# Kernel tuning notes

Hardware: AMD Instinct MI355X
Metric: run time of the kernel (lower is better)

The kernel has to match this reference:

```python
import jax, jax.numpy as jnp
import numpy as np


def setup_inputs() -> dict:
    key = jax.random.key(0)
    k1, k2 = jax.random.split(key)
    N = 2_000_000
    rotation = jax.random.normal(k1, (N, 3, 3), dtype=jnp.float32)
    # learned parameter: eye(3) + 0.001 * randn(3,3)
    mat = jnp.eye(3, dtype=jnp.float32) + 0.001 * jax.random.normal(k2, (3, 3), dtype=jnp.float32)
    return {"rotation": rotation, "mat": mat}


def reference(rotation, mat):
    # new_mat[n] = rotation[n] @ mat   (mat broadcast over the batch)
    new_mat = jnp.einsum('nab,bc->nac', rotation, mat)
    # batched 3x3 SVD; polar orthogonal factor U @ V^T
    U, S, Vh = jnp.linalg.svd(new_mat, full_matrices=False)
    out = jnp.einsum('nab,nbc->nac', U, Vh)  # Vh is already V^T
    logdet = jnp.zeros((rotation.shape[0],), dtype=rotation.dtype)
    return out, logdet
```

## Files before the change

### kernel.cpp

```cpp
#include <hip/hip_runtime.h>
#include <math.h>

constexpr int BLOCK = 256;

__global__ __launch_bounds__(BLOCK) void polar3x3_kernel(
    const float* __restrict__ rot,
    const float* __restrict__ mat,
    float* __restrict__ outq,
    float* __restrict__ logdet,
    int N)
{
    __shared__ float lds[BLOCK * 9];
    const int tid = threadIdx.x;
    const long long base = (long long)blockIdx.x * BLOCK;
    const int rem = (int)(N - base);
    const int nmat = rem < BLOCK ? rem : BLOCK;
    const int nflt = nmat * 9;
    const int nv4 = nflt >> 2;

    const float* gsrc = rot + base * 9;
    {
        const float4* g4 = (const float4*)gsrc;
        float4* l4 = (float4*)lds;
        for (int i = tid; i < nv4; i += BLOCK) l4[i] = g4[i];
        for (int i = (nv4 << 2) + tid; i < nflt; i += BLOCK) lds[i] = gsrc[i];
    }

    const float m0=mat[0], m1=mat[1], m2=mat[2], m3=mat[3], m4=mat[4],
                m5=mat[5], m6=mat[6], m7=mat[7], m8=mat[8];
    const double dM = (double)m0*((double)m4*m8-(double)m5*m7)
                    - (double)m1*((double)m3*m8-(double)m5*m6)
                    + (double)m2*((double)m3*m7-(double)m4*m6);
    __syncthreads();

    const bool active = tid < nmat;
    float x0=1.f,x1=0.f,x2=0.f,x3=0.f,x4=1.f,x5=0.f,x6=0.f,x7=0.f,x8=1.f;
    float detA = 1.f;

    if (active) {
        const float* r = &lds[tid * 9];
        const float r0=r[0],r1=r[1],r2=r[2],r3=r[3],r4=r[4],r5=r[5],r6=r[6],r7=r[7],r8=r[8];
        const double dR = (double)r0*((double)r4*r8-(double)r5*r7)
                        - (double)r1*((double)r3*r8-(double)r5*r6)
                        + (double)r2*((double)r3*r7-(double)r4*r6);
        detA = (float)(dR * dM);
        x0=fmaf(r0,m0,fmaf(r1,m3,r2*m6));
        x1=fmaf(r0,m1,fmaf(r1,m4,r2*m7));
        x2=fmaf(r0,m2,fmaf(r1,m5,r2*m8));
        x3=fmaf(r3,m0,fmaf(r4,m3,r5*m6));
        x4=fmaf(r3,m1,fmaf(r4,m4,r5*m7));
        x5=fmaf(r3,m2,fmaf(r4,m5,r5*m8));
        x6=fmaf(r6,m0,fmaf(r7,m3,r8*m6));
        x7=fmaf(r6,m1,fmaf(r7,m4,r8*m7));
        x8=fmaf(r6,m2,fmaf(r7,m5,r8*m8));
    }

    #pragma unroll
    for (int it = 0; it < 5; ++it) {
        const float c0=fmaf(x4,x8,-x5*x7), c1=fmaf(x5,x6,-x3*x8), c2=fmaf(x3,x7,-x4*x6);
        const float c3=fmaf(x2,x7,-x1*x8), c4=fmaf(x0,x8,-x2*x6), c5=fmaf(x1,x6,-x0*x7);
        const float c6=fmaf(x1,x5,-x2*x4), c7=fmaf(x2,x3,-x0*x5), c8=fmaf(x0,x4,-x1*x3);
        const float det = (it==0) ? detA : fmaf(x0,c0,fmaf(x1,c1,x2*c2));
        const float adet = fmaxf(fabsf(det), 1e-30f);
        float nX2, nC2;
        { const float a=fmaf(x1,x1,x0*x0), b=fmaf(x3,x3,x2*x2),
                      e=fmaf(x5,x5,x4*x4), d=fmaf(x7,x7,x6*x6);
          nX2=(a+b)+(e+fmaf(x8,x8,d)); }
        { const float a=fmaf(c1,c1,c0*c0), b=fmaf(c3,c3,c2*c2),
                      e=fmaf(c5,c5,c4*c4), d=fmaf(c7,c7,c6*c6);
          nC2=(a+b)+(e+fmaf(c8,c8,d)); }
        const float h  = __builtin_amdgcn_rsqf(adet);
        const float pr = __builtin_amdgcn_sqrtf(__builtin_amdgcn_sqrtf(
                             nC2*__builtin_amdgcn_rcpf(nX2)));
        const float qr = __builtin_amdgcn_sqrtf(__builtin_amdgcn_sqrtf(
                             nX2*__builtin_amdgcn_rcpf(nC2)));
        const float s = 0.5f*pr*h;
        const float t = copysignf(0.5f*qr*h, det);
        x0=fmaf(s,x0,t*c0); x1=fmaf(s,x1,t*c1); x2=fmaf(s,x2,t*c2);
        x3=fmaf(s,x3,t*c3); x4=fmaf(s,x4,t*c4); x5=fmaf(s,x5,t*c5);
        x6=fmaf(s,x6,t*c6); x7=fmaf(s,x7,t*c7); x8=fmaf(s,x8,t*c8);
    }
    {
        const float c0=fmaf(x4,x8,-x5*x7), c1=fmaf(x5,x6,-x3*x8), c2=fmaf(x3,x7,-x4*x6);
        const float c3=fmaf(x2,x7,-x1*x8), c4=fmaf(x0,x8,-x2*x6), c5=fmaf(x1,x6,-x0*x7);
        const float c6=fmaf(x1,x5,-x2*x4), c7=fmaf(x2,x3,-x0*x5), c8=fmaf(x0,x4,-x1*x3);
        const float det = fmaf(x0,c0,fmaf(x1,c1,x2*c2));
        const float t = 0.5f*__builtin_amdgcn_rcpf(det);
        x0=fmaf(0.5f,x0,t*c0); x1=fmaf(0.5f,x1,t*c1); x2=fmaf(0.5f,x2,t*c2);
        x3=fmaf(0.5f,x3,t*c3); x4=fmaf(0.5f,x4,t*c4); x5=fmaf(0.5f,x5,t*c5);
        x6=fmaf(0.5f,x6,t*c6); x7=fmaf(0.5f,x7,t*c7); x8=fmaf(0.5f,x8,t*c8);
    }

    if (active) {
        float* w = &lds[tid * 9];
        w[0]=x0; w[1]=x1; w[2]=x2; w[3]=x3; w[4]=x4;
        w[5]=x5; w[6]=x6; w[7]=x7; w[8]=x8;
    }
    __syncthreads();

    float* gdst = outq + base * 9;
    {
        float4* g4 = (float4*)gdst;
        const float4* l4 = (const float4*)lds;
        for (int i = tid; i < nv4; i += BLOCK) g4[i] = l4[i];
        for (int i = (nv4 << 2) + tid; i < nflt; i += BLOCK) gdst[i] = lds[i];
    }

    if (base + tid < N) logdet[base + tid] = 0.0f;
}

extern "C" void kernel_launch(void* const* d_in, const int* in_sizes, int n_in,
                              void* d_out, int out_size, void* d_ws, size_t ws_size,
                              hipStream_t stream) {
    const float* rot = (const float*)d_in[0];
    const float* mat = (const float*)d_in[1];
    float* out = (float*)d_out;
    const int N = in_sizes[0] / 9;
    float* logdet = out + (long long)N * 9;
    const int nblocks = (N + BLOCK - 1) / BLOCK;
    polar3x3_kernel<<<nblocks, BLOCK, 0, stream>>>(rot, mat, out, logdet, N);
}
```

Measured before the change: 138.8 us.

## Use per-wave LDS staging, fp32 determinants, and drop final Newton step

Each wave now stages its own 64 matrices through LDS with wave barriers instead of block-wide __syncthreads. Tail handling is removed, so it assumes N is a multiple of 64. Determinants are computed in fp32, falling back to fp64 only when the value is near zero. The per-iteration scaling needs fewer transcendental calls, and the final unscaled Newton iteration is removed, which may cost accuracy.

New measurement: 145.6 us. +4.9%, slower.

```diff
diff --git a/kernel.cpp b/kernel.cpp
--- a/kernel.cpp
+++ b/kernel.cpp
@@ -2,6 +2,7 @@
 #include <math.h>
 
 constexpr int BLOCK = 256;
+constexpr int WAVE  = 64;
 
 __global__ __launch_bounds__(BLOCK) void polar3x3_kernel(
     const float* __restrict__ rot,
@@ -11,49 +12,52 @@
     int N)
 {
     __shared__ float lds[BLOCK * 9];
-    const int tid = threadIdx.x;
-    const long long base = (long long)blockIdx.x * BLOCK;
-    const int rem = (int)(N - base);
-    const int nmat = rem < BLOCK ? rem : BLOCK;
-    const int nflt = nmat * 9;
-    const int nv4 = nflt >> 2;
+    const int tid  = threadIdx.x;
+    const int lane = tid & 63;
+    const int wave = tid >> 6;
+    const long long matBase = (long long)blockIdx.x * BLOCK + (long long)wave * WAVE;
+    if (matBase >= N) return;
 
-    const float* gsrc = rot + base * 9;
+    float* wlds = &lds[wave * (WAVE * 9)];
+
     {
-        const float4* g4 = (const float4*)gsrc;
-        float4* l4 = (float4*)lds;
-        for (int i = tid; i < nv4; i += BLOCK) l4[i] = g4[i];
-        for (int i = (nv4 << 2) + tid; i < nflt; i += BLOCK) lds[i] = gsrc[i];
+        const float4* g4 = (const float4*)(rot + matBase * 9);
+        float4* l4 = (float4*)wlds;
+        l4[lane]      = g4[lane];
+        l4[lane + 64] = g4[lane + 64];
+        if (lane < 16) l4[lane + 128] = g4[lane + 128];
     }
+    __builtin_amdgcn_wave_barrier();
 
     const float m0=mat[0], m1=mat[1], m2=mat[2], m3=mat[3], m4=mat[4],
                 m5=mat[5], m6=mat[6], m7=mat[7], m8=mat[8];
-    const double dM = (double)m0*((double)m4*m8-(double)m5*m7)
-                    - (double)m1*((double)m3*m8-(double)m5*m6)
-                    + (double)m2*((double)m3*m7-(double)m4*m6);
-    __syncthreads();
+    const float dMf = fmaf(m0, fmaf(m4,m8,-m5*m7),
+                      fmaf(-m1, fmaf(m3,m8,-m5*m6),
+                           m2 * fmaf(m3,m7,-m4*m6)));
 
-    const bool active = tid < nmat;
-    float x0=1.f,x1=0.f,x2=0.f,x3=0.f,x4=1.f,x5=0.f,x6=0.f,x7=0.f,x8=1.f;
-    float detA = 1.f;
+    const float* r = &wlds[lane * 9];
+    const float r0=r[0],r1=r[1],r2=r[2],r3=r[3],r4=r[4],r5=r[5],r6=r[6],r7=r[7],r8=r[8];
 
-    if (active) {
-        const float* r = &lds[tid * 9];
-        const float r0=r[0],r1=r[1],r2=r[2],r3=r[3],r4=r[4],r5=r[5],r6=r[6],r7=r[7],r8=r[8];
+    float dRf = fmaf(r0, fmaf(r4,r8,-r5*r7),
+               fmaf(-r1, fmaf(r3,r8,-r5*r6),
+                    r2 * fmaf(r3,r7,-r4*r6)));
+    if (__builtin_expect(fabsf(dRf) < 1e-3f, 0)) {
         const double dR = (double)r0*((double)r4*r8-(double)r5*r7)
                         - (double)r1*((double)r3*r8-(double)r5*r6)
                         + (double)r2*((double)r3*r7-(double)r4*r6);
-        detA = (float)(dR * dM);
-        x0=fmaf(r0,m0,fmaf(r1,m3,r2*m6));
-        x1=fmaf(r0,m1,fmaf(r1,m4,r2*m7));
-        x2=fmaf(r0,m2,fmaf(r1,m5,r2*m8));
-        x3=fmaf(r3,m0,fmaf(r4,m3,r5*m6));
-        x4=fmaf(r3,m1,fmaf(r4,m4,r5*m7));
-        x5=fmaf(r3,m2,fmaf(r4,m5,r5*m8));
-        x6=fmaf(r6,m0,fmaf(r7,m3,r8*m6));
-        x7=fmaf(r6,m1,fmaf(r7,m4,r8*m7));
-        x8=fmaf(r6,m2,fmaf(r7,m5,r8*m8));
+        dRf = (float)dR;
     }
+    const float detA = dRf * dMf;
+
+    float x0=fmaf(r0,m0,fmaf(r1,m3,r2*m6));
+    float x1=fmaf(r0,m1,fmaf(r1,m4,r2*m7));
+    float x2=fmaf(r0,m2,fmaf(r1,m5,r2*m8));
+    float x3=fmaf(r3,m0,fmaf(r4,m3,r5*m6));
+    float x4=fmaf(r3,m1,fmaf(r4,m4,r5*m7));
+    float x5=fmaf(r3,m2,fmaf(r4,m5,r5*m8));
+    float x6=fmaf(r6,m0,fmaf(r7,m3,r8*m6));
+    float x7=fmaf(r6,m1,fmaf(r7,m4,r8*m7));
+    float x8=fmaf(r6,m2,fmaf(r7,m5,r8*m8));
 
     #pragma unroll
     for (int it = 0; it < 5; ++it) {
@@ -61,7 +65,7 @@
         const float c3=fmaf(x2,x7,-x1*x8), c4=fmaf(x0,x8,-x2*x6), c5=fmaf(x1,x6,-x0*x7);
         const float c6=fmaf(x1,x5,-x2*x4), c7=fmaf(x2,x3,-x0*x5), c8=fmaf(x0,x4,-x1*x3);
         const float det = (it==0) ? detA : fmaf(x0,c0,fmaf(x1,c1,x2*c2));
-        const float adet = fmaxf(fabsf(det), 1e-30f);
+        const float adet = fmaxf(fabsf(det), 1e-12f);
         float nX2, nC2;
         { const float a=fmaf(x1,x1,x0*x0), b=fmaf(x3,x3,x2*x2),
                       e=fmaf(x5,x5,x4*x4), d=fmaf(x7,x7,x6*x6);
@@ -69,44 +73,33 @@
         { const float a=fmaf(c1,c1,c0*c0), b=fmaf(c3,c3,c2*c2),
                       e=fmaf(c5,c5,c4*c4), d=fmaf(c7,c7,c6*c6);
           nC2=(a+b)+(e+fmaf(c8,c8,d)); }
+        const float rn = __builtin_amdgcn_rsqf(nX2);
+        const float sc = __builtin_amdgcn_sqrtf(nC2);
+        const float sp = __builtin_amdgcn_sqrtf(sc * rn);
         const float h  = __builtin_amdgcn_rsqf(adet);
-        const float pr = __builtin_amdgcn_sqrtf(__builtin_amdgcn_sqrtf(
-                             nC2*__builtin_amdgcn_rcpf(nX2)));
-        const float qr = __builtin_amdgcn_sqrtf(__builtin_amdgcn_sqrtf(
-                             nX2*__builtin_amdgcn_rcpf(nC2)));
-        const float s = 0.5f*pr*h;
-        const float t = copysignf(0.5f*qr*h, det);
+        const float s  = 0.5f * sp * h;
+        const float t  = copysignf(0.5f * h * __builtin_amdgcn_rcpf(sp), det);
         x0=fmaf(s,x0,t*c0); x1=fmaf(s,x1,t*c1); x2=fmaf(s,x2,t*c2);
         x3=fmaf(s,x3,t*c3); x4=fmaf(s,x4,t*c4); x5=fmaf(s,x5,t*c5);
         x6=fmaf(s,x6,t*c6); x7=fmaf(s,x7,t*c7); x8=fmaf(s,x8,t*c8);
     }
+
     {
-        const float c0=fmaf(x4,x8,-x5*x7), c1=fmaf(x5,x6,-x3*x8), c2=fmaf(x3,x7,-x4*x6);
-        const float c3=fmaf(x2,x7,-x1*x8), c4=fmaf(x0,x8,-x2*x6), c5=fmaf(x1,x6,-x0*x7);
-        const float c6=fmaf(x1,x5,-x2*x4), c7=fmaf(x2,x3,-x0*x5), c8=fmaf(x0,x4,-x1*x3);
-        const float det = fmaf(x0,c0,fmaf(x1,c1,x2*c2));
-        const float t = 0.5f*__builtin_amdgcn_rcpf(det);
-        x0=fmaf(0.5f,x0,t*c0); x1=fmaf(0.5f,x1,t*c1); x2=fmaf(0.5f,x2,t*c2);
-        x3=fmaf(0.5f,x3,t*c3); x4=fmaf(0.5f,x4,t*c4); x5=fmaf(0.5f,x5,t*c5);
-        x6=fmaf(0.5f,x6,t*c6); x7=fmaf(0.5f,x7,t*c7); x8=fmaf(0.5f,x8,t*c8);
-    }
-
-    if (active) {
-        float* w = &lds[tid * 9];
+        float* w = &wlds[lane * 9];
         w[0]=x0; w[1]=x1; w[2]=x2; w[3]=x3; w[4]=x4;
         w[5]=x5; w[6]=x6; w[7]=x7; w[8]=x8;
     }
-    __syncthreads();
+    __builtin_amdgcn_wave_barrier();
 
-    float* gdst = outq + base * 9;
     {
-        float4* g4 = (float4*)gdst;
-        const float4* l4 = (const float4*)lds;
-        for (int i = tid; i < nv4; i += BLOCK) g4[i] = l4[i];
-        for (int i = (nv4 << 2) + tid; i < nflt; i += BLOCK) gdst[i] = lds[i];
+        float4* o4 = (float4*)(outq + matBase * 9);
+        const float4* l4 = (const float4*)wlds;
+        o4[lane]      = l4[lane];
+        o4[lane + 64] = l4[lane + 64];
+        if (lane < 16) o4[lane + 128] = l4[lane + 128];
     }
 
-    if (base + tid < N) logdet[base + tid] = 0.0f;
+    logdet[matBase + lane] = 0.0f;
 }
 
 extern "C" void kernel_launch(void* const* d_in, const int* in_sizes, int n_in,
```
